# Performance work log

Hardware: AMD Instinct MI355X
Metric: run time of the kernel (lower is better)

Reference implementation:

```python
import jax, jax.numpy as jnp
import numpy as np

N_NODES = 100000
N_EDGES = 1600000
N_GRAPHS = 64
IN_DIM = 397


def setup_inputs() -> dict:
    key = jax.random.key(0)
    ks = jax.random.split(key, 16)
    x = jax.random.normal(ks[0], (N_NODES, IN_DIM), dtype=jnp.float32)
    edge_index = jax.random.randint(ks[1], (2, N_EDGES), 0, N_NODES, dtype=jnp.int64)
    batch = jnp.sort(jax.random.randint(ks[2], (N_NODES,), 0, N_GRAPHS, dtype=jnp.int64))

    def lin(k, fan_in, fan_out):
        s = 1.0 / np.sqrt(fan_in)
        return jax.random.uniform(k, (fan_in, fan_out), jnp.float32, -s, s)

    return {
        "x": x, "edge_index": edge_index, "batch": batch,
        "W1": lin(ks[3], IN_DIM, 128), "b1": jnp.zeros((128,), jnp.float32),
        "W2": lin(ks[4], 128, 128),   "b2": jnp.zeros((128,), jnp.float32),
        "W3": lin(ks[5], 128, 64),    "b3": jnp.zeros((64,), jnp.float32),
        "Wh1": lin(ks[6], 64, 32),    "bh1": jnp.zeros((32,), jnp.float32),
        "Wh2": lin(ks[7], 32, 1),     "bh2": jnp.zeros((1,), jnp.float32),
    }


def _gcn_conv(x, src, dst, deg_isqrt, W, b, n_nodes):
    # PyG GCNConv: linear first, then sym-normalized aggregation with self-loops.
    xw = x @ W  # [N, out]
    norm = deg_isqrt[src] * deg_isqrt[dst]  # [E]
    agg = jax.ops.segment_sum(xw[src] * norm[:, None], dst, num_segments=n_nodes)
    # self-loop contribution: deg^{-1/2}[i] * deg^{-1/2}[i] * xw[i]
    agg = agg + xw * (deg_isqrt * deg_isqrt)[:, None]
    return agg + b


def reference(x, edge_index, batch, W1, b1, W2, b2, W3, b3, Wh1, bh1, Wh2, bh2):
    n_nodes = x.shape[0]
    src, dst = edge_index[0], edge_index[1]
    # degree after adding self-loops (edge weight 1), counted at destination
    deg = jax.ops.segment_sum(jnp.ones_like(src, dtype=x.dtype), dst,
                              num_segments=n_nodes) + 1.0
    deg_isqrt = jax.lax.rsqrt(deg)

    h = jax.nn.relu(_gcn_conv(x, src, dst, deg_isqrt, W1, b1, n_nodes))
    # dropout p=0.2 -> identity in eval
    h = jax.nn.relu(_gcn_conv(h, src, dst, deg_isqrt, W2, b2, n_nodes))
    h = jax.nn.relu(_gcn_conv(h, src, dst, deg_isqrt, W3, b3, n_nodes))

    # global max pool over graphs in the batch
    g = jax.ops.segment_max(h, batch, num_segments=N_GRAPHS)  # [G, 64]

    # MLP head (Dropout(0.3) identity in eval)
    g = jax.nn.relu(g @ Wh1 + bh1)
    out = g @ Wh2 + bh2  # [G, 1]
    return out.squeeze(-1)
```

## Files before the change

kernel.cpp:

```cpp
#include <hip/hip_runtime.h>
#include <hip/hip_bf16.h>
#include <hip/hip_fp16.h>


typedef float f4u __attribute__((ext_vector_type(4), aligned(4)));
typedef unsigned short u16;
typedef u16 u16x8 __attribute__((ext_vector_type(8)));
typedef short bf16x8 __attribute__((ext_vector_type(8)));
typedef float f32x4 __attribute__((ext_vector_type(4)));
typedef _Float16 f16;
typedef f16 f16x8 __attribute__((ext_vector_type(8)));

__device__ __forceinline__ u16 bf16_rne(float f) {
    unsigned u = __float_as_uint(f);
    return (u16)((u + 0x7FFF + ((u >> 16) & 1)) >> 16);
}
__device__ __forceinline__ float bf16_f(u16 h) {
    return __uint_as_float(((unsigned)h) << 16);
}

__global__ void deg_count_kernel(const int* __restrict__ ei, int* __restrict__ cnt, int E) {
    int e = blockIdx.x * 256 + threadIdx.x;
    if (e < E) atomicAdd(&cnt[ei[E + e]], 1);
}

__global__ void deg_fin_kernel(const int* __restrict__ cnt, float* __restrict__ disq, int N) {
    int i = blockIdx.x * 256 + threadIdx.x;
    if (i < N) disq[i] = rsqrtf((float)cnt[i] + 1.0f);
}

__global__ void scan_pass1(const int* __restrict__ cnt, int* __restrict__ bsum, int N) {
    __shared__ int s[256];
    int t = threadIdx.x;
    int base = blockIdx.x * 1024 + t * 4;
    int sum = 0;
    #pragma unroll
    for (int j = 0; j < 4; ++j) { int idx = base + j; if (idx < N) sum += cnt[idx]; }
    s[t] = sum; __syncthreads();
    for (int off = 128; off; off >>= 1) {
        if (t < off) s[t] += s[t + off];
        __syncthreads();
    }
    if (t == 0) bsum[blockIdx.x] = s[0];
}

__global__ void scan_pass2(const int* __restrict__ bsum, int* __restrict__ boff,
                           int nchunks, int* __restrict__ rp, int N, int E) {
    __shared__ int s[256];
    int t = threadIdx.x;
    int v = (t < nchunks) ? bsum[t] : 0;
    s[t] = v; __syncthreads();
    for (int off = 1; off < 256; off <<= 1) {
        int x = (t >= off) ? s[t - off] : 0;
        __syncthreads();
        s[t] += x;
        __syncthreads();
    }
    boff[t] = s[t] - v;
    if (t == 0) rp[N] = E;
}

__global__ void scan_pass3(const int* __restrict__ cnt, const int* __restrict__ boff,
                           int* __restrict__ rp, int N) {
    __shared__ int s[256];
    int t = threadIdx.x;
    int base = blockIdx.x * 1024 + t * 4;
    int v[4]; int sum = 0;
    #pragma unroll
    for (int j = 0; j < 4; ++j) { int idx = base + j; v[j] = (idx < N) ? cnt[idx] : 0; sum += v[j]; }
    s[t] = sum; __syncthreads();
    for (int off = 1; off < 256; off <<= 1) {
        int x = (t >= off) ? s[t - off] : 0;
        __syncthreads();
        s[t] += x;
        __syncthreads();
    }
    int ex = s[t] - sum + boff[blockIdx.x];
    #pragma unroll
    for (int j = 0; j < 4; ++j) { int idx = base + j; if (idx < N) { rp[idx] = ex; ex += v[j]; } }
}

__global__ void scatter_kernel(const int* __restrict__ ei, const float* __restrict__ disq,
                               const int* __restrict__ rp, int* __restrict__ fill,
                               int2* __restrict__ esw, int E) {
    int e = blockIdx.x * 256 + threadIdx.x;
    if (e >= E) return;
    int s = ei[e];
    int d = ei[E + e];
    int pos = rp[d] + atomicAdd(&fill[d], 1);
    int2 p; p.x = s; p.y = __float_as_int(disq[s] * disq[d]);
    esw[pos] = p;
}

__global__ void cvtw_kernel(const float* __restrict__ W, u16* __restrict__ Wthi,
                            u16* __restrict__ Wtlo, int K, int KP, int BN) {
    int idx = blockIdx.x * 256 + threadIdx.x;
    if (idx >= KP * BN) return;
    int c = idx / KP;
    int k = idx % KP;
    float v = (k < K) ? W[(long)k * BN + c] : 0.f;
    u16 h = bf16_rne(v);
    Wthi[idx] = h;
    Wtlo[idx] = bf16_rne(v - bf16_f(h));
}

template <int BN, bool AFP32>
__global__ __launch_bounds__(256) void mfma_gemm(
    const float* __restrict__ Af, const u16* __restrict__ Ahi,
    const u16* __restrict__ Alo, const u16* __restrict__ Wthi,
    const u16* __restrict__ Wtlo, f16* __restrict__ Xh, int N, int K, int KP)
{
    constexpr int FC = BN / 16;
    __shared__ u16 Ah[128 * 40];
    __shared__ u16 Al[128 * 40];
    __shared__ u16 Wh[BN * 40];
    __shared__ u16 Wl[BN * 40];
    const int tid = threadIdx.x;
    const int w = tid >> 6;
    const int l = tid & 63;
    const int l15 = l & 15;
    const int koff = (l >> 4) * 8;
    const long base = (long)blockIdx.x * 128;

    f32x4 acc[2][FC];
    #pragma unroll
    for (int i = 0; i < 2; ++i)
        #pragma unroll
        for (int j = 0; j < FC; ++j) acc[i][j] = (f32x4){0.f, 0.f, 0.f, 0.f};

    for (int k0 = 0; k0 < KP; k0 += 32) {
        #pragma unroll
        for (int it = 0; it < 2; ++it) {
            int i2 = tid + it * 256;
            int r = i2 >> 2;
            int kq = (i2 & 3) * 8;
            long row = base + r;
            u16x8 hv = (u16x8)0, lv = (u16x8)0;
            if constexpr (AFP32) {
                int rem = K - (k0 + kq);
                if (row < N && rem > 0) {
                    const float* ap = &Af[row * (long)K + k0 + kq];
                    float f[8];
                    if (rem >= 8) {
                        f4u v0 = *(const f4u*)ap;
                        f4u v1 = *(const f4u*)(ap + 4);
                        f[0] = v0.x; f[1] = v0.y; f[2] = v0.z; f[3] = v0.w;
                        f[4] = v1.x; f[5] = v1.y; f[6] = v1.z; f[7] = v1.w;
                    } else {
                        #pragma unroll
                        for (int j = 0; j < 8; ++j) f[j] = (j < rem) ? ap[j] : 0.f;
                    }
                    #pragma unroll
                    for (int j = 0; j < 8; ++j) {
                        u16 h = bf16_rne(f[j]);
                        hv[j] = h;
                        lv[j] = bf16_rne(f[j] - bf16_f(h));
                    }
                }
            } else {
                if (row < N) {
                    hv = *(const u16x8*)&Ahi[row * (long)K + k0 + kq];
                    lv = *(const u16x8*)&Alo[row * (long)K + k0 + kq];
                }
            }
            *(u16x8*)&Ah[r * 40 + kq] = hv;
            *(u16x8*)&Al[r * 40 + kq] = lv;
        }
        #pragma unroll
        for (int it = 0; it < (BN * 4) / 256; ++it) {
            int i2 = tid + it * 256;
            int c = i2 >> 2;
            int kq = (i2 & 3) * 8;
            *(u16x8*)&Wh[c * 40 + kq] = *(const u16x8*)&Wthi[(long)c * KP + k0 + kq];
            *(u16x8*)&Wl[c * 40 + kq] = *(const u16x8*)&Wtlo[(long)c * KP + k0 + kq];
        }
        __syncthreads();
        bf16x8 ah[2], al[2];
        #pragma unroll
        for (int fr = 0; fr < 2; ++fr) {
            int ar = (w * 32 + fr * 16 + l15) * 40 + koff;
            ah[fr] = *(const bf16x8*)&Ah[ar];
            al[fr] = *(const bf16x8*)&Al[ar];
        }
        #pragma unroll
        for (int fc = 0; fc < FC; ++fc) {
            int wr = (fc * 16 + l15) * 40 + koff;
            bf16x8 bh = *(const bf16x8*)&Wh[wr];
            bf16x8 bl = *(const bf16x8*)&Wl[wr];
            #pragma unroll
            for (int fr = 0; fr < 2; ++fr) {
                acc[fr][fc] = __builtin_amdgcn_mfma_f32_16x16x32_bf16(ah[fr], bh, acc[fr][fc], 0, 0, 0);
                acc[fr][fc] = __builtin_amdgcn_mfma_f32_16x16x32_bf16(al[fr], bh, acc[fr][fc], 0, 0, 0);
                acc[fr][fc] = __builtin_amdgcn_mfma_f32_16x16x32_bf16(ah[fr], bl, acc[fr][fc], 0, 0, 0);
            }
        }
        __syncthreads();
    }
    #pragma unroll
    for (int fr = 0; fr < 2; ++fr) {
        #pragma unroll
        for (int fc = 0; fc < FC; ++fc) {
            int col = fc * 16 + l15;
            #pragma unroll
            for (int reg = 0; reg < 4; ++reg) {
                long row = base + w * 32 + fr * 16 + (l >> 4) * 4 + reg;
                if (row < N) Xh[row * BN + col] = (f16)acc[fr][fc][reg];
            }
        }
    }
}

template <int C, bool B16OUT>
__global__ __launch_bounds__(256) void agg_kernel(
    const f16* __restrict__ xh, const float* __restrict__ disq,
    const int* __restrict__ rp, const int2* __restrict__ esw,
    const float* __restrict__ bias, float* __restrict__ h,
    u16* __restrict__ hhi, u16* __restrict__ hlo, int N)
{
    int i = blockIdx.x * 4 + (threadIdx.x >> 6);
    if (i >= N) return;
    int lane = threadIdx.x & 63;
    int e0 = rp[i], e1 = rp[i + 1];
    constexpr int LPE = C / 8;
    constexpr int EPW = 64 / LPE;
    int sub = lane / LPE;
    int col = lane % LPE;
    const f16x8* x8 = (const f16x8*)xh;

    float a0[8], a1[8];
    #pragma unroll
    for (int j = 0; j < 8; ++j) { a0[j] = 0.f; a1[j] = 0.f; }

    int e = e0 + sub;
    for (; e + EPW < e1; e += 2 * EPW) {
        int2 p0 = esw[e];
        int2 p1 = esw[e + EPW];
        f16x8 v0 = x8[(long)p0.x * LPE + col];
        f16x8 v1 = x8[(long)p1.x * LPE + col];
        float w0 = __int_as_float(p0.y), w1 = __int_as_float(p1.y);
        #pragma unroll
        for (int j = 0; j < 8; ++j) {
            a0[j] += (float)v0[j] * w0;
            a1[j] += (float)v1[j] * w1;
        }
    }
    for (; e < e1; e += EPW) {
        int2 p0 = esw[e];
        f16x8 v0 = x8[(long)p0.x * LPE + col];
        float w0 = __int_as_float(p0.y);
        #pragma unroll
        for (int j = 0; j < 8; ++j) a0[j] += (float)v0[j] * w0;
    }
    #pragma unroll
    for (int j = 0; j < 8; ++j) a0[j] += a1[j];
    #pragma unroll
    for (int m = LPE; m < 64; m <<= 1) {
        #pragma unroll
        for (int j = 0; j < 8; ++j) a0[j] += __shfl_xor(a0[j], m, 64);
    }
    if (sub == 0) {
        float ds = disq[i];
        float ws = ds * ds;
        f16x8 v = x8[(long)i * LPE + col];
        const float* bp = bias + col * 8;
        float4 b0 = *(const float4*)bp;
        float4 b1 = *(const float4*)(bp + 4);
        float bb[8] = {b0.x, b0.y, b0.z, b0.w, b1.x, b1.y, b1.z, b1.w};
        float o[8];
        #pragma unroll
        for (int j = 0; j < 8; ++j)
            o[j] = fmaxf(a0[j] + (float)v[j] * ws + bb[j], 0.f);
        if constexpr (B16OUT) {
            u16x8 oh, ol;
            #pragma unroll
            for (int j = 0; j < 8; ++j) {
                u16 hh = bf16_rne(o[j]);
                oh[j] = hh;
                ol[j] = bf16_rne(o[j] - bf16_f(hh));
            }
            *(u16x8*)&hhi[(long)i * C + col * 8] = oh;
            *(u16x8*)&hlo[(long)i * C + col * 8] = ol;
        } else {
            float4 v0 = {o[0], o[1], o[2], o[3]};
            float4 v1 = {o[4], o[5], o[6], o[7]};
            *(float4*)&h[(long)i * C + col * 8] = v0;
            *(float4*)&h[(long)i * C + col * 8 + 4] = v1;
        }
    }
}

__global__ __launch_bounds__(256) void pool_kernel(
    const float* __restrict__ h, const int* __restrict__ batch,
    float* __restrict__ g, int N)
{
    int c = threadIdx.x & 63;
    int slot = threadIdx.x >> 6;
    int base = blockIdx.x * 512;
    int end = base + 512; if (end > N) end = N;
    int cur = -1; float m = 0.f;
    for (int n = base + slot; n < end; n += 4) {
        int b = batch[n];
        float v = h[(long)n * 64 + c];
        if (b != cur) {
            if (cur >= 0) atomicMax((int*)&g[cur * 64 + c], __float_as_int(m));
            cur = b; m = v;
        } else {
            m = fmaxf(m, v);
        }
    }
    if (cur >= 0) atomicMax((int*)&g[cur * 64 + c], __float_as_int(m));
}

__global__ void head_kernel(const float* __restrict__ g, const float* __restrict__ Wh1,
                            const float* __restrict__ bh1, const float* __restrict__ Wh2,
                            const float* __restrict__ bh2, float* __restrict__ out, int G) {
    int r = threadIdx.x;
    if (r >= G) return;
    float hid[32];
    #pragma unroll
    for (int j = 0; j < 32; ++j) {
        float s = bh1[j];
        for (int k = 0; k < 64; ++k) s += g[r * 64 + k] * Wh1[k * 32 + j];
        hid[j] = fmaxf(s, 0.f);
    }
    float o = bh2[0];
    #pragma unroll
    for (int j = 0; j < 32; ++j) o += hid[j] * Wh2[j];
    out[r] = o;
}

extern "C" void kernel_launch(void* const* d_in, const int* in_sizes, int n_in,
                              void* d_out, int out_size, void* d_ws, size_t ws_size,
                              hipStream_t stream) {
    const float* x   = (const float*)d_in[0];
    const int*   ei  = (const int*)d_in[1];
    const int*   bat = (const int*)d_in[2];
    const float* W1  = (const float*)d_in[3];
    const float* b1  = (const float*)d_in[4];
    const float* W2  = (const float*)d_in[5];
    const float* b2  = (const float*)d_in[6];
    const float* W3  = (const float*)d_in[7];
    const float* b3  = (const float*)d_in[8];
    const float* Wh1 = (const float*)d_in[9];
    const float* bh1 = (const float*)d_in[10];
    const float* Wh2 = (const float*)d_in[11];
    const float* bh2 = (const float*)d_in[12];
    float* out = (float*)d_out;

    const int N = in_sizes[2];
    const int E = in_sizes[1] / 2;
    const int K1 = in_sizes[0] / N;
    const int G = out_size;
    const int KP1 = ((K1 + 31) / 32) * 32;

    char* wsp = (char*)d_ws;
    size_t off = 0;
    auto alloc = [&](size_t bytes) -> void* {
        void* p = wsp + off;
        off = (off + bytes + 255) & ~(size_t)255;
        return p;
    };
    int*   cnt   = (int*)alloc((size_t)N * 4);
    float* disq  = (float*)alloc((size_t)N * 4);
    int*   rp    = (int*)alloc((size_t)(N + 1) * 4);
    int*   bsum  = (int*)alloc(256 * 4);
    int*   boff  = (int*)alloc(256 * 4);
    int2*  esw   = (int2*)alloc((size_t)E * 8);
    u16*   Wt1hi = (u16*)alloc((size_t)KP1 * 128 * 2);
    u16*   Wt1lo = (u16*)alloc((size_t)KP1 * 128 * 2);
    u16*   Wt2hi = (u16*)alloc((size_t)128 * 128 * 2);
    u16*   Wt2lo = (u16*)alloc((size_t)128 * 128 * 2);
    u16*   Wt3hi = (u16*)alloc((size_t)128 * 64 * 2);
    u16*   Wt3lo = (u16*)alloc((size_t)128 * 64 * 2);
    f16*   Xh    = (f16*)alloc((size_t)N * 128 * 2);
    u16*   Hhi   = (u16*)alloc((size_t)N * 128 * 2);
    u16*   Hlo   = (u16*)alloc((size_t)N * 128 * 2);
    float* h3    = (float*)alloc((size_t)N * 64 * 4);
    float* g     = (float*)alloc((size_t)G * 64 * 4);

    const int nchunks = (N + 1023) / 1024;

    (void)hipMemsetAsync(cnt, 0, (size_t)N * 4, stream);
    deg_count_kernel<<<(E + 255) / 256, 256, 0, stream>>>(ei, cnt, E);
    deg_fin_kernel<<<(N + 255) / 256, 256, 0, stream>>>(cnt, disq, N);
    scan_pass1<<<nchunks, 256, 0, stream>>>(cnt, bsum, N);
    scan_pass2<<<1, 256, 0, stream>>>(bsum, boff, nchunks, rp, N, E);
    scan_pass3<<<nchunks, 256, 0, stream>>>(cnt, boff, rp, N);
    (void)hipMemsetAsync(cnt, 0, (size_t)N * 4, stream);
    scatter_kernel<<<(E + 255) / 256, 256, 0, stream>>>(ei, disq, rp, cnt, esw, E);

    cvtw_kernel<<<(KP1 * 128 + 255) / 256, 256, 0, stream>>>(W1, Wt1hi, Wt1lo, K1, KP1, 128);
    cvtw_kernel<<<(128 * 128 + 255) / 256, 256, 0, stream>>>(W2, Wt2hi, Wt2lo, 128, 128, 128);
    cvtw_kernel<<<(128 * 64 + 255) / 256, 256, 0, stream>>>(W3, Wt3hi, Wt3lo, 128, 128, 64);

    int gblocks = (N + 127) / 128;
    int ablocks = (N + 3) / 4;
    mfma_gemm<128, true><<<gblocks, 256, 0, stream>>>(x, nullptr, nullptr, Wt1hi, Wt1lo, Xh, N, K1, KP1);
    agg_kernel<128, true><<<ablocks, 256, 0, stream>>>(Xh, disq, rp, esw, b1, nullptr, Hhi, Hlo, N);
    mfma_gemm<128, false><<<gblocks, 256, 0, stream>>>(nullptr, Hhi, Hlo, Wt2hi, Wt2lo, Xh, N, 128, 128);
    agg_kernel<128, true><<<ablocks, 256, 0, stream>>>(Xh, disq, rp, esw, b2, nullptr, Hhi, Hlo, N);
    mfma_gemm<64, false><<<gblocks, 256, 0, stream>>>(nullptr, Hhi, Hlo, Wt3hi, Wt3lo, Xh, N, 128, 128);
    agg_kernel<64, false><<<ablocks, 256, 0, stream>>>(Xh, disq, rp, esw, b3, h3, nullptr, nullptr, N);
    (void)hipMemsetAsync(g, 0, (size_t)G * 64 * 4, stream);
    pool_kernel<<<(N + 511) / 512, 256, 0, stream>>>(h3, bat, g, N);
    head_kernel<<<1, 64, 0, stream>>>(g, Wh1, bh1, Wh2, bh2, out, G);
}
```

Baseline: 547.1 us.

## Load GEMM A fragments directly into registers and use 512-thread blocks

The GEMM kernel stops staging the A tile through shared memory. Each lane now loads its own MFMA A fragment (hi/lo bf16 split) straight from global memory into registers. Blocks grow to 8 waves of 16 rows each instead of 4 waves of 32 rows, and only W stays in LDS. This removes LDS writes and reads for A and frees shared memory, at the cost of less per-wave reuse of the B fragments, which are now read from LDS once per 16 rows instead of once per 32. The per-lane global loads are strided by row (8 elements per lane), which may coalesce less well.

```diff
diff --git a/kernel.cpp b/kernel.cpp
--- a/kernel.cpp
+++ b/kernel.cpp
@@ -105,14 +105,12 @@
 }
 
 template <int BN, bool AFP32>
-__global__ __launch_bounds__(256) void mfma_gemm(
+__global__ __launch_bounds__(512) void mfma_gemm(
     const float* __restrict__ Af, const u16* __restrict__ Ahi,
     const u16* __restrict__ Alo, const u16* __restrict__ Wthi,
     const u16* __restrict__ Wtlo, f16* __restrict__ Xh, int N, int K, int KP)
 {
     constexpr int FC = BN / 16;
-    __shared__ u16 Ah[128 * 40];
-    __shared__ u16 Al[128 * 40];
     __shared__ u16 Wh[BN * 40];
     __shared__ u16 Wl[BN * 40];
     const int tid = threadIdx.x;
@@ -121,25 +119,30 @@
     const int l15 = l & 15;
     const int koff = (l >> 4) * 8;
     const long base = (long)blockIdx.x * 128;
-
-    f32x4 acc[2][FC];
-    #pragma unroll
-    for (int i = 0; i < 2; ++i)
-        #pragma unroll
-        for (int j = 0; j < FC; ++j) acc[i][j] = (f32x4){0.f, 0.f, 0.f, 0.f};
+    const long arow = base + w * 16 + l15;
+    const bool rowOK = (arow < N);
+
+    f32x4 acc[FC];
+    #pragma unroll
+    for (int j = 0; j < FC; ++j) acc[j] = (f32x4){0.f, 0.f, 0.f, 0.f};
 
     for (int k0 = 0; k0 < KP; k0 += 32) {
-        #pragma unroll
-        for (int it = 0; it < 2; ++it) {
-            int i2 = tid + it * 256;
-            int r = i2 >> 2;
-            int kq = (i2 & 3) * 8;
-            long row = base + r;
+        {
+            int i2 = tid;
+            if (i2 < BN * 4) {
+                int c = i2 >> 2;
+                int kq = (i2 & 3) * 8;
+                *(u16x8*)&Wh[c * 40 + kq] = *(const u16x8*)&Wthi[(long)c * KP + k0 + kq];
+                *(u16x8*)&Wl[c * 40 + kq] = *(const u16x8*)&Wtlo[(long)c * KP + k0 + kq];
+            }
+        }
+        bf16x8 ah, al;
+        {
             u16x8 hv = (u16x8)0, lv = (u16x8)0;
             if constexpr (AFP32) {
-                int rem = K - (k0 + kq);
-                if (row < N && rem > 0) {
-                    const float* ap = &Af[row * (long)K + k0 + kq];
+                int rem = K - (k0 + koff);
+                if (rowOK && rem > 0) {
+                    const float* ap = &Af[arow * (long)K + k0 + koff];
                     float f[8];
                     if (rem >= 8) {
                         f4u v0 = *(const f4u*)ap;
@@ -158,54 +161,33 @@
                     }
                 }
             } else {
-                if (row < N) {
-                    hv = *(const u16x8*)&Ahi[row * (long)K + k0 + kq];
-                    lv = *(const u16x8*)&Alo[row * (long)K + k0 + kq];
+                if (rowOK) {
+                    hv = *(const u16x8*)&Ahi[arow * (long)K + k0 + koff];
+                    lv = *(const u16x8*)&Alo[arow * (long)K + k0 + koff];
                 }
             }
-            *(u16x8*)&Ah[r * 40 + kq] = hv;
-            *(u16x8*)&Al[r * 40 + kq] = lv;
-        }
-        #pragma unroll
-        for (int it = 0; it < (BN * 4) / 256; ++it) {
-            int i2 = tid + it * 256;
-            int c = i2 >> 2;
-            int kq = (i2 & 3) * 8;
-            *(u16x8*)&Wh[c * 40 + kq] = *(const u16x8*)&Wthi[(long)c * KP + k0 + kq];
-            *(u16x8*)&Wl[c * 40 + kq] = *(const u16x8*)&Wtlo[(long)c * KP + k0 + kq];
-        }
-        __syncthreads();
-        bf16x8 ah[2], al[2];
-        #pragma unroll
-        for (int fr = 0; fr < 2; ++fr) {
-            int ar = (w * 32 + fr * 16 + l15) * 40 + koff;
-            ah[fr] = *(const bf16x8*)&Ah[ar];
-            al[fr] = *(const bf16x8*)&Al[ar];
-        }
+            ah = __builtin_bit_cast(bf16x8, hv);
+            al = __builtin_bit_cast(bf16x8, lv);
+        }
+        __syncthreads();
         #pragma unroll
         for (int fc = 0; fc < FC; ++fc) {
             int wr = (fc * 16 + l15) * 40 + koff;
             bf16x8 bh = *(const bf16x8*)&Wh[wr];
             bf16x8 bl = *(const bf16x8*)&Wl[wr];
-            #pragma unroll
-            for (int fr = 0; fr < 2; ++fr) {
-                acc[fr][fc] = __builtin_amdgcn_mfma_f32_16x16x32_bf16(ah[fr], bh, acc[fr][fc], 0, 0, 0);
-                acc[fr][fc] = __builtin_amdgcn_mfma_f32_16x16x32_bf16(al[fr], bh, acc[fr][fc], 0, 0, 0);
-                acc[fr][fc] = __builtin_amdgcn_mfma_f32_16x16x32_bf16(ah[fr], bl, acc[fr][fc], 0, 0, 0);
-            }
-        }
-        __syncthreads();
-    }
-    #pragma unroll
-    for (int fr = 0; fr < 2; ++fr) {
-        #pragma unroll
-        for (int fc = 0; fc < FC; ++fc) {
-            int col = fc * 16 + l15;
-            #pragma unroll
-            for (int reg = 0; reg < 4; ++reg) {
-                long row = base + w * 32 + fr * 16 + (l >> 4) * 4 + reg;
-                if (row < N) Xh[row * BN + col] = (f16)acc[fr][fc][reg];
-            }
+            acc[fc] = __builtin_amdgcn_mfma_f32_16x16x32_bf16(ah, bh, acc[fc], 0, 0, 0);
+            acc[fc] = __builtin_amdgcn_mfma_f32_16x16x32_bf16(al, bh, acc[fc], 0, 0, 0);
+            acc[fc] = __builtin_amdgcn_mfma_f32_16x16x32_bf16(ah, bl, acc[fc], 0, 0, 0);
+        }
+        __syncthreads();
+    }
+    #pragma unroll
+    for (int fc = 0; fc < FC; ++fc) {
+        int col = fc * 16 + l15;
+        #pragma unroll
+        for (int reg = 0; reg < 4; ++reg) {
+            long row = base + w * 16 + (l >> 4) * 4 + reg;
+            if (row < N) Xh[row * BN + col] = (f16)acc[fc][reg];
         }
     }
 }
@@ -395,11 +377,11 @@
 
     int gblocks = (N + 127) / 128;
     int ablocks = (N + 3) / 4;
-    mfma_gemm<128, true><<<gblocks, 256, 0, stream>>>(x, nullptr, nullptr, Wt1hi, Wt1lo, Xh, N, K1, KP1);
+    mfma_gemm<128, true><<<gblocks, 512, 0, stream>>>(x, nullptr, nullptr, Wt1hi, Wt1lo, Xh, N, K1, KP1);
     agg_kernel<128, true><<<ablocks, 256, 0, stream>>>(Xh, disq, rp, esw, b1, nullptr, Hhi, Hlo, N);
-    mfma_gemm<128, false><<<gblocks, 256, 0, stream>>>(nullptr, Hhi, Hlo, Wt2hi, Wt2lo, Xh, N, 128, 128);
+    mfma_gemm<128, false><<<gblocks, 512, 0, stream>>>(nullptr, Hhi, Hlo, Wt2hi, Wt2lo, Xh, N, 128, 128);
     agg_kernel<128, true><<<ablocks, 256, 0, stream>>>(Xh, disq, rp, esw, b2, nullptr, Hhi, Hlo, N);
-    mfma_gemm<64, false><<<gblocks, 256, 0, stream>>>(nullptr, Hhi, Hlo, Wt3hi, Wt3lo, Xh, N, 128, 128);
+    mfma_gemm<64, false><<<gblocks, 512, 0, stream>>>(nullptr, Hhi, Hlo, Wt3hi, Wt3lo, Xh, N, 128, 128);
     agg_kernel<64, false><<<ablocks, 256, 0, stream>>>(Xh, disq, rp, esw, b3, h3, nullptr, nullptr, N);
     (void)hipMemsetAsync(g, 0, (size_t)G * 64 * 4, stream);
     pool_kernel<<<(N + 511) / 512, 256, 0, stream>>>(h3, bat, g, N);
```

Result: faster. 531.4 us (-2.9%).
